# Optimization experiments

Measured on AMD Instinct MI355X. Metric: run time of the kernel, lower is better.

## Reference

```python
import jax, jax.numpy as jnp
import numpy as np

MOMENTUM = 0.8
EPSILON = 1e-05


def setup_inputs() -> dict:
    key = jax.random.key(0)
    k_x, = jax.random.split(key, 1)
    bs, C, H, W = 32, 3, 512, 512
    x = jax.random.normal(k_x, (bs, C, H, W), dtype=jnp.float32)
    gamma = jnp.ones((C,), dtype=jnp.float32)
    beta = jnp.zeros((C,), dtype=jnp.float32)
    running_mean = jnp.zeros((C,), dtype=jnp.float32)
    running_var = jnp.ones((C,), dtype=jnp.float32)
    return {"x": x, "gamma": gamma, "beta": beta,
            "running_mean": running_mean, "running_var": running_var}


def reference(x, gamma, beta, running_mean, running_var):
    # --- get_mean_var_fourier: batched ifft2 -> real -> per-channel stats ---
    # sx: [bs, C, H, W] real part of 2D inverse FFT per (batch, channel)
    sx = jnp.fft.ifft2(x, axes=(-2, -1)).real.astype(x.dtype)
    # per-channel mean/var over (batch, H, W) -- matches reshape(C,-1) stats
    mean = jnp.mean(sx, axis=(0, 2, 3))                      # [C]
    var = jnp.mean((sx - mean[None, :, None, None]) ** 2, axis=(0, 2, 3))  # [C]
    # --- running-stat update (training mode) ---
    rm = running_mean * MOMENTUM + (1.0 - MOMENTUM) * mean   # [C]
    rv = running_var * MOMENTUM + (1.0 - MOMENTUM) * var     # [C]
    # --- single-pass channel-wise affine normalize (fused) ---
    inv_std = 1.0 / jnp.sqrt(rv + EPSILON)                   # [C]
    out = (gamma * inv_std)[None, :, None, None] * (x - rm[None, :, None, None]) \
          + beta[None, :, None, None]
    return out
```

## Files before the change

### kernel.cpp

```cpp
#include <hip/hip_runtime.h>
#include <math.h>

#define BS 32
#define CH 3
#define HH 512
#define WW 512
#define HWSZ (HH * WW)
#define MOMENTUM 0.8
#define EPSILON 1e-5


constexpr int BPP = 16;
constexpr int F4_PER_BLOCK = HWSZ / 4 / BPP;
constexpr int STAT_THREADS = 256;
constexpr int F4_PER_THREAD = F4_PER_BLOCK / STAT_THREADS;
constexpr int BATCH = 4;
constexpr int NBATCH = F4_PER_THREAD / BATCH;
constexpr int NBLOCKS = BS * CH * BPP;

__global__ __launch_bounds__(STAT_THREADS) void stats_kernel(
    const float* __restrict__ x, float4* __restrict__ partials) {
    const int plane = blockIdx.x / BPP;
    const int blk   = blockIdx.x % BPP;
    const float* __restrict__ base = x + (size_t)plane * HWSZ;
    const int tid = threadIdx.x;
    const int start4 = blk * F4_PER_BLOCK;

    float s1 = 0.f, s2 = 0.f, s3 = 0.f;

    for (int nb = 0; nb < NBATCH; ++nb) {
        float4 a[BATCH], p1[BATCH], p2[BATCH];
#pragma unroll
        for (int j = 0; j < BATCH; ++j) {
            const int o = (start4 + tid + (nb * BATCH + j) * STAT_THREADS) * 4;
            const bool w0 = (o & (WW - 1)) == 0;
            const int q1 = (HWSZ + 508 - o) & (HWSZ - 1);
            const int q2 = (HWSZ + (w0 ? 0 : 512) - o) & (HWSZ - 1);
            a[j]  = *reinterpret_cast<const float4*>(base + o);
            p1[j] = *reinterpret_cast<const float4*>(base + q1);
            p2[j] = *reinterpret_cast<const float4*>(base + q2);
        }
#pragma unroll
        for (int j = 0; j < BATCH; ++j) {
            const float4 a_ = a[j], p1_ = p1[j], p2_ = p2[j];
            s2 += a_.x * a_.x + a_.y * a_.y + a_.z * a_.z + a_.w * a_.w;
            s3 += a_.x * p2_.x + a_.y * p1_.w + a_.z * p1_.z + a_.w * p1_.y;
            const int o = (start4 + tid + (nb * BATCH + j) * STAT_THREADS) * 4;
            if (o == 0) s1 += a_.x;
        }
    }

#pragma unroll
    for (int off = 32; off > 0; off >>= 1) {
        s1 += __shfl_down(s1, off);
        s2 += __shfl_down(s2, off);
        s3 += __shfl_down(s3, off);
    }
    __shared__ float red[3][4];
    const int lane = tid & 63, wv = tid >> 6;
    if (lane == 0) { red[0][wv] = s1; red[1][wv] = s2; red[2][wv] = s3; }
    __syncthreads();
    if (tid == 0) {
        float4 p;
        p.x = red[0][0] + red[0][1] + red[0][2] + red[0][3];
        p.y = red[1][0] + red[1][1] + red[1][2] + red[1][3];
        p.z = red[2][0] + red[2][1] + red[2][2] + red[2][3];
        p.w = 0.f;
        partials[blockIdx.x] = p;
    }
}

__global__ __launch_bounds__(256) void finalize_kernel(
    const float4* __restrict__ partials,
    const float* __restrict__ gamma, const float* __restrict__ beta,
    const float* __restrict__ rmean, const float* __restrict__ rvar,
    float* __restrict__ ss) {
    const int c = blockIdx.x;
    const int tid = threadIdx.x;
    const int per_c = BS * BPP;
    double t1 = 0.0, t2 = 0.0, t3 = 0.0;
    for (int k = tid; k < per_c; k += 256) {
        const int b = k / BPP, blk = k % BPP;
        const float4 p = partials[(b * CH + c) * BPP + blk];
        t1 += (double)p.x; t2 += (double)p.y; t3 += (double)p.z;
    }
#pragma unroll
    for (int off = 32; off > 0; off >>= 1) {
        t1 += __shfl_down(t1, off);
        t2 += __shfl_down(t2, off);
        t3 += __shfl_down(t3, off);
    }
    __shared__ double red[3][4];
    const int lane = tid & 63, wv = tid >> 6;
    if (lane == 0) { red[0][wv] = t1; red[1][wv] = t2; red[2][wv] = t3; }
    __syncthreads();
    if (tid == 0) {
        const double S1 = red[0][0] + red[0][1] + red[0][2] + red[0][3];
        const double S2 = red[1][0] + red[1][1] + red[1][2] + red[1][3];
        const double S3 = red[2][0] + red[2][1] + red[2][2] + red[2][3];
        const double N = (double)BS * (double)HWSZ;
        const double mean = S1 / N;
        const double ex2  = (S2 + S3) / (2.0 * N * (double)HWSZ);
        const double var  = ex2 - mean * mean;
        const double rm = (double)rmean[c] * MOMENTUM + (1.0 - MOMENTUM) * mean;
        const double rv = (double)rvar[c]  * MOMENTUM + (1.0 - MOMENTUM) * var;
        const double inv_std = 1.0 / sqrt(rv + EPSILON);
        const float scale = (float)((double)gamma[c] * inv_std);
        const float shift = (float)((double)beta[c] - (double)scale * rm);
        ss[c * 2 + 0] = scale;
        ss[c * 2 + 1] = shift;
    }
}

__global__ __launch_bounds__(256) void norm_kernel(
    const float* __restrict__ x, const float* __restrict__ ss,
    float* __restrict__ out) {
    float sc[CH], sh[CH];
#pragma unroll
    for (int c = 0; c < CH; ++c) { sc[c] = ss[c * 2]; sh[c] = ss[c * 2 + 1]; }
    const int n4 = BS * CH * HWSZ / 4;
    const int stride = gridDim.x * blockDim.x;
    for (int i4 = blockIdx.x * blockDim.x + threadIdx.x; i4 < n4; i4 += stride) {
        const int c = (i4 >> 16) % CH;
        const float4 v = reinterpret_cast<const float4*>(x)[i4];
        const float s = sc[c], t = sh[c];
        float4 o;
        o.x = fmaf(v.x, s, t);
        o.y = fmaf(v.y, s, t);
        o.z = fmaf(v.z, s, t);
        o.w = fmaf(v.w, s, t);
        reinterpret_cast<float4*>(out)[i4] = o;
    }
}

extern "C" void kernel_launch(void* const* d_in, const int* in_sizes, int n_in,
                              void* d_out, int out_size, void* d_ws, size_t ws_size,
                              hipStream_t stream) {
    const float* x     = (const float*)d_in[0];
    const float* gamma = (const float*)d_in[1];
    const float* beta  = (const float*)d_in[2];
    const float* rmean = (const float*)d_in[3];
    const float* rvar  = (const float*)d_in[4];
    float* out = (float*)d_out;

    float4* partials = (float4*)d_ws;
    float*  ss = (float*)((char*)d_ws + NBLOCKS * 16);

    stats_kernel<<<NBLOCKS, STAT_THREADS, 0, stream>>>(x, partials);
    finalize_kernel<<<CH, 256, 0, stream>>>(partials, gamma, beta, rmean, rvar, ss);
    norm_kernel<<<2048, 256, 0, stream>>>(x, ss, out);
}
```

Measured before the change: 67.63 us.

## Exploit conjugate symmetry to halve rows read by stats kernel

The stats kernel now covers only rows 0..255 of each plane (16 rows per block across 16 blocks), while still loading the mirrored-index partner elements. The squared terms of those partners are added to the sum, and cross products are doubled for rows other than row 0. A separate tail step processes the self-paired middle row 256. This cuts the primary loads in the stats pass roughly in half, at the cost of more per-element arithmetic and special-case handling of row 0 and row 256.

Measured after the change: 59.92 us. 1.13x faster.

```diff
diff --git a/kernel.cpp b/kernel.cpp
--- a/kernel.cpp
+++ b/kernel.cpp
@@ -11,9 +11,9 @@
 
 
 constexpr int BPP = 16;
-constexpr int F4_PER_BLOCK = HWSZ / 4 / BPP;
+constexpr int ROWS_PER_BLK = 16;
 constexpr int STAT_THREADS = 256;
-constexpr int F4_PER_THREAD = F4_PER_BLOCK / STAT_THREADS;
+constexpr int F4_PER_THREAD = ROWS_PER_BLK * (WW / 4) / STAT_THREADS;
 constexpr int BATCH = 4;
 constexpr int NBATCH = F4_PER_THREAD / BATCH;
 constexpr int NBLOCKS = BS * CH * BPP;
@@ -24,7 +24,7 @@
     const int blk   = blockIdx.x % BPP;
     const float* __restrict__ base = x + (size_t)plane * HWSZ;
     const int tid = threadIdx.x;
-    const int start4 = blk * F4_PER_BLOCK;
+    const int h0  = blk * ROWS_PER_BLK;
 
     float s1 = 0.f, s2 = 0.f, s3 = 0.f;
 
@@ -32,8 +32,11 @@
         float4 a[BATCH], p1[BATCH], p2[BATCH];
 #pragma unroll
         for (int j = 0; j < BATCH; ++j) {
-            const int o = (start4 + tid + (nb * BATCH + j) * STAT_THREADS) * 4;
-            const bool w0 = (o & (WW - 1)) == 0;
+            const int idx  = tid + (nb * BATCH + j) * STAT_THREADS;
+            const int r    = idx >> 7;
+            const int col4 = idx & 127;
+            const int o    = ((h0 + r) << 9) + (col4 << 2);
+            const bool w0  = (col4 == 0);
             const int q1 = (HWSZ + 508 - o) & (HWSZ - 1);
             const int q2 = (HWSZ + (w0 ? 0 : 512) - o) & (HWSZ - 1);
             a[j]  = *reinterpret_cast<const float4*>(base + o);
@@ -42,12 +45,29 @@
         }
 #pragma unroll
         for (int j = 0; j < BATCH; ++j) {
+            const int idx = tid + (nb * BATCH + j) * STAT_THREADS;
+            const int h   = h0 + (idx >> 7);
             const float4 a_ = a[j], p1_ = p1[j], p2_ = p2[j];
-            s2 += a_.x * a_.x + a_.y * a_.y + a_.z * a_.z + a_.w * a_.w;
-            s3 += a_.x * p2_.x + a_.y * p1_.w + a_.z * p1_.z + a_.w * p1_.y;
-            const int o = (start4 + tid + (nb * BATCH + j) * STAT_THREADS) * 4;
-            if (o == 0) s1 += a_.x;
+            const float asq = a_.x * a_.x + a_.y * a_.y + a_.z * a_.z + a_.w * a_.w;
+            const float qsq = p1_.x * p1_.x + p1_.y * p1_.y + p1_.z * p1_.z + p1_.w * p1_.w;
+            const float prd = a_.x * p2_.x + a_.y * p1_.w + a_.z * p1_.z + a_.w * p1_.y;
+            const float two = (h == 0) ? 0.f : 1.f;
+            s2 += asq + two * qsq;
+            s3 += (h == 0 ? 1.f : 2.f) * prd;
+            if (h == 0 && idx == 0) s1 += a_.x;
         }
+    }
+
+    if (blk == 0 && tid < 128) {
+        const int o  = 256 * WW + tid * 4;
+        const bool w0 = (tid == 0);
+        const int q1 = (HWSZ + 508 - o) & (HWSZ - 1);
+        const int q2 = (HWSZ + (w0 ? 0 : 512) - o) & (HWSZ - 1);
+        const float4 a_  = *reinterpret_cast<const float4*>(base + o);
+        const float4 p1_ = *reinterpret_cast<const float4*>(base + q1);
+        const float4 p2_ = *reinterpret_cast<const float4*>(base + q2);
+        s2 += a_.x * a_.x + a_.y * a_.y + a_.z * a_.z + a_.w * a_.w;
+        s3 += a_.x * p2_.x + a_.y * p1_.w + a_.z * p1_.z + a_.w * p1_.y;
     }
 
 #pragma unroll
```
